# Kernel optimization log

Hardware: AMD Instinct MI355X
Metric: run time of the kernel (lower is better)

The kernel has to match this reference:

```python
import jax, jax.numpy as jnp
import numpy as np

N_HEADS = 16
HIDDEN = 1024
HEAD = HIDDEN // N_HEADS


def setup_inputs() -> dict:
    key = jax.random.key(0)
    ks = jax.random.split(key, 11)
    B, S, H = 2, 2048, HIDDEN
    s = 1.0 / np.sqrt(H)
    return {
        "query": jax.random.normal(ks[0], (B, S, H), jnp.float32),
        "key": jax.random.normal(ks[1], (B, S, H), jnp.float32),
        "value": jax.random.normal(ks[2], (B, S, H), jnp.float32),
        "Wq": jax.random.normal(ks[3], (H, H), jnp.float32) * s,
        "bq": jnp.zeros((H,), jnp.float32),
        "Wk": jax.random.normal(ks[4], (H, H), jnp.float32) * s,
        "bk": jnp.zeros((H,), jnp.float32),
        "Wv": jax.random.normal(ks[5], (H, H), jnp.float32) * s,
        "bv": jnp.zeros((H,), jnp.float32),
        "Wo": jax.random.normal(ks[6], (H, H), jnp.float32) * s,
        "bo": jnp.zeros((H,), jnp.float32),
    }


def reference(query, key, value, Wq, bq, Wk, bk, Wv, bv, Wo, bo):
    B, Sq, H = query.shape
    Sk = key.shape[1]
    # QKV projections, split heads: [B, n_heads, S, head]
    q = (query @ Wq + bq).reshape(B, Sq, N_HEADS, HEAD).transpose(0, 2, 1, 3)
    k = (key @ Wk + bk).reshape(B, Sk, N_HEADS, HEAD).transpose(0, 2, 1, 3)
    v = (value @ Wv + bv).reshape(B, Sk, N_HEADS, HEAD).transpose(0, 2, 1, 3)
    # scaled dot-product attention (no mask, dropout p=0)
    scores = jnp.einsum("bhqd,bhkd->bhqk", q, k) / np.sqrt(HEAD).astype(np.float32)
    attn = jax.nn.softmax(scores, axis=-1)
    out = jnp.einsum("bhqk,bhkd->bhqd", attn, v)
    out = out.transpose(0, 2, 1, 3).reshape(B, Sq, H)
    return out @ Wo + bo
```

## Files before the change

### kernel.cpp

```cpp
#include <hip/hip_runtime.h>
#include <hip/hip_bf16.h>
#include <stdint.h>

typedef unsigned short u16;
typedef short bf16x8 __attribute__((ext_vector_type(8)));
typedef float f32x4 __attribute__((ext_vector_type(4)));

#define DEVI static __device__ __forceinline__

#if __has_builtin(__builtin_amdgcn_exp2f)
#define EXP2F(x) __builtin_amdgcn_exp2f(x)
#else
#define EXP2F(x) exp2f(x)
#endif

DEVI u16 f2bf(float f) {
  union { float f; uint32_t u; } v; v.f = f;
  uint32_t u = v.u;
  u += 0x7fffu + ((u >> 16) & 1u);
  return (u16)(u >> 16);
}
DEVI uint32_t pk2bf(float lo, float hi) {
  __hip_bfloat162 h = __float22bfloat162_rn(float2{lo, hi});
  union { __hip_bfloat162 h; uint32_t u; } v; v.h = h; return v.u;
}

DEVI void async16(const void* g, const void* l) {
  __builtin_amdgcn_global_load_lds(
      (const __attribute__((address_space(1))) void*)g,
      (__attribute__((address_space(3))) void*)l, 16, 0, 0);
}

DEVI f32x4 mfma16(bf16x8 a, bf16x8 b, f32x4 c) {
  return __builtin_amdgcn_mfma_f32_16x16x32_bf16(a, b, c, 0, 0, 0);
}

#define CSC 0.18033688011112042f

__global__ void convx(const float* __restrict__ q, const float* __restrict__ k,
                      const float* __restrict__ v, u16* __restrict__ out) {
  const int z = blockIdx.y;
  const float* src = (z == 0) ? q : (z == 1) ? k : v;
  const int i = (blockIdx.x * 256 + threadIdx.x) * 4;
  float4 f = *(const float4*)(src + i);
  ushort4 o;
  o.x = f2bf(f.x); o.y = f2bf(f.y); o.z = f2bf(f.z); o.w = f2bf(f.w);
  *(ushort4*)(out + (size_t)z * 4194304 + i) = o;
}

__global__ void transw(const float* __restrict__ Wq, const float* __restrict__ Wk,
                       const float* __restrict__ Wv, const float* __restrict__ Wo,
                       u16* __restrict__ WT) {
  __shared__ u16 tile[64 * 68];
  const int z = blockIdx.z;
  const float* W = (z == 0) ? Wq : (z == 1) ? Wk : (z == 2) ? Wv : Wo;
  u16* out = WT + (size_t)z * 1048576;
  const int R0 = blockIdx.y * 64, C0 = blockIdx.x * 64;
  const int t = threadIdx.x;
#pragma unroll
  for (int it = 0; it < 16; ++it) {
    int j = it * 256 + t;
    int r = j >> 6, c = j & 63;
    tile[r * 68 + c] = f2bf(W[(size_t)(R0 + r) * 1024 + C0 + c]);
  }
  __syncthreads();
#pragma unroll
  for (int it = 0; it < 16; ++it) {
    int j = it * 256 + t;
    int c = j >> 6, r = j & 63;
    out[(size_t)(C0 + c) * 1024 + R0 + r] = tile[r * 68 + c];
  }
}

__global__ __launch_bounds__(256, 3)
void qkv_gemm(const u16* __restrict__ XB, const u16* __restrict__ WT,
              const float* __restrict__ bq, const float* __restrict__ bk,
              const float* __restrict__ bv,
              u16* __restrict__ QN, u16* __restrict__ KN, u16* __restrict__ VT) {
  __shared__ u16 smem[16896];
  u16* lA = smem;
  u16* lB = smem + 8192;
  const int z = blockIdx.y;
  const u16* A  = XB + (size_t)z * 4194304;
  const u16* Bt = WT + (size_t)z * 1048576;
  const float* bias = (z == 0) ? bq : (z == 1) ? bk : bv;
  const int T = blockIdx.x;
  const int m0 = (T & 31) * 128, n0 = (T >> 5) * 128;
  const int t = threadIdx.x, lane = t & 63, w = t >> 6;
  const int quad = lane >> 4, l16 = lane & 15;
  const int wm = (w & 1) * 64, wn = (w >> 1) * 64;

  f32x4 acc[4][4] = {};
  for (int kt = 0; kt < 16; ++kt) {
    const int k0 = kt * 64;
#pragma unroll
    for (int it = 0; it < 4; ++it) {
      int i = it * 256 + t;
      int r = i >> 3, cc = i & 7, c = cc ^ (r & 7);
      async16(A + (size_t)(m0 + r) * 1024 + k0 + c * 8, &lA[i * 8]);
      async16(Bt + (size_t)(n0 + r) * 1024 + k0 + c * 8, &lB[i * 8]);
    }
    __syncthreads();
#pragma unroll
    for (int ks = 0; ks < 2; ++ks) {
      bf16x8 af[4], bfr[4];
#pragma unroll
      for (int rt = 0; rt < 4; ++rt) {
        int row = wm + rt * 16 + l16;
        af[rt] = *(const bf16x8*)&lA[row * 64 + ((ks * 4 + quad) ^ (row & 7)) * 8];
      }
#pragma unroll
      for (int ct = 0; ct < 4; ++ct) {
        int row = wn + ct * 16 + l16;
        bfr[ct] = *(const bf16x8*)&lB[row * 64 + ((ks * 4 + quad) ^ (row & 7)) * 8];
      }
#pragma unroll
      for (int rt = 0; rt < 4; ++rt)
#pragma unroll
        for (int ct = 0; ct < 4; ++ct)
          acc[rt][ct] = mfma16(bfr[ct], af[rt], acc[rt][ct]);
    }
    __syncthreads();
  }

  if (z < 2) {
    const float scl = (z == 0) ? CSC : 1.0f;
#pragma unroll
    for (int rt = 0; rt < 4; ++rt) {
      int sl = wm + rt * 16 + l16;
#pragma unroll
      for (int ct = 0; ct < 4; ++ct) {
        int nb = wn + ct * 16 + quad * 4;
        float4 b4 = *(const float4*)&bias[n0 + nb];
        ushort4 pk;
        pk.x = f2bf((acc[rt][ct][0] + b4.x) * scl);
        pk.y = f2bf((acc[rt][ct][1] + b4.y) * scl);
        pk.z = f2bf((acc[rt][ct][2] + b4.z) * scl);
        pk.w = f2bf((acc[rt][ct][3] + b4.w) * scl);
        *(ushort4*)&smem[sl * 132 + nb] = pk;
      }
    }
    __syncthreads();
    u16* out = (z == 0) ? QN : KN;
#pragma unroll
    for (int p = 0; p < 8; ++p) {
      int idx = p * 256 + t;
      int row = idx >> 4, chunk = idx & 15;
      *(bf16x8*)&out[(size_t)(m0 + row) * 1024 + n0 + chunk * 8] =
          *(const bf16x8*)&smem[row * 132 + chunk * 8];
    }
  } else {
#pragma unroll
    for (int rt = 0; rt < 4; ++rt) {
      int sl = wm + rt * 16 + l16;
#pragma unroll
      for (int ct = 0; ct < 4; ++ct) {
        int nb = wn + ct * 16 + quad * 4;
        float4 b4 = *(const float4*)&bias[n0 + nb];
        smem[(nb + 0) * 132 + sl] = f2bf(acc[rt][ct][0] + b4.x);
        smem[(nb + 1) * 132 + sl] = f2bf(acc[rt][ct][1] + b4.y);
        smem[(nb + 2) * 132 + sl] = f2bf(acc[rt][ct][2] + b4.z);
        smem[(nb + 3) * 132 + sl] = f2bf(acc[rt][ct][3] + b4.w);
      }
    }
    __syncthreads();
    const int bb = m0 >> 11, sb = m0 & 2047;
#pragma unroll
    for (int p = 0; p < 8; ++p) {
      int idx = p * 256 + t;
      int dl = idx >> 4, chunk = idx & 15;
      int ncol = n0 + dl, hh = ncol >> 6, dd = ncol & 63;
      *(bf16x8*)&VT[((size_t)((bb * 16 + hh) * 64 + dd)) * 2048 + sb + chunk * 8] =
          *(const bf16x8*)&smem[dl * 132 + chunk * 8];
    }
  }
}

__global__ __launch_bounds__(512, 4)
void attn10(const u16* __restrict__ QN, const u16* __restrict__ KN,
            const u16* __restrict__ VT, u16* __restrict__ AO) {
  __shared__ u16 lK[4][64 * 64];
  __shared__ u16 lV[4][64 * 64];
  const int qt0 = blockIdx.x, h = blockIdx.y, b = blockIdx.z;
  const int t = threadIdx.x, lane = t & 63, w = t >> 6;
  const int quad = lane >> 4, l16 = lane & 15;
  const u16* Qg = QN + ((size_t)(b * 2048 + qt0 * 128)) * 1024 + h * 64;
  const u16* Kg = KN + ((size_t)b * 2048) * 1024 + h * 64;
  const u16* Vg = VT + ((size_t)((b * 16 + h) * 64)) * 2048;

  const int sr_r = t >> 3;
  const int sg_r = (sr_r & 0x23) | ((sr_r & 8) << 1) | ((sr_r & 4) << 1) |
                   ((sr_r & 16) >> 2);
  const int sc_c = (t & 7) ^ (sr_r & 7);

  bf16x8 qf[2];
#pragma unroll
  for (int ks = 0; ks < 2; ++ks)
    qf[ks] = *(const bf16x8*)(Qg + (size_t)(w * 16 + l16) * 1024 + ks * 32 + quad * 8);

  const bf16x8 ones = {0x3F80, 0x3F80, 0x3F80, 0x3F80,
                       0x3F80, 0x3F80, 0x3F80, 0x3F80};

  async16(Kg + (size_t)sg_r * 1024 + sc_c * 8, &lK[0][t * 8]);
  async16(Vg + (size_t)sr_r * 2048 + sc_c * 8, &lV[0][t * 8]);
  async16(Kg + (size_t)(64 + sg_r) * 1024 + sc_c * 8, &lK[1][t * 8]);
  async16(Vg + (size_t)sr_r * 2048 + 64 + sc_c * 8, &lV[1][t * 8]);

  f32x4 o[4] = {};
  f32x4 ls = {};

  for (int kt = 0; kt < 32; ++kt) {
    if (kt + 2 < 32) {
      const int kb = (kt + 2) * 64;
      const int nb2 = (kt + 2) & 3;
      async16(Kg + (size_t)(kb + sg_r) * 1024 + sc_c * 8, &lK[nb2][t * 8]);
      async16(Vg + (size_t)sr_r * 2048 + kb + sc_c * 8, &lV[nb2][t * 8]);
    }
    if (kt < 30)       asm volatile("s_waitcnt vmcnt(4)" ::: "memory");
    else if (kt == 30) asm volatile("s_waitcnt vmcnt(2)" ::: "memory");
    else               asm volatile("s_waitcnt vmcnt(0)" ::: "memory");
    __builtin_amdgcn_s_barrier();
    __builtin_amdgcn_sched_barrier(0);

    const int cur = kt & 3;

    f32x4 sc[4];
    __builtin_amdgcn_s_setprio(1);
#pragma unroll
    for (int st = 0; st < 4; ++st) {
      int row = st * 16 + l16;
      bf16x8 kf0 = *(const bf16x8*)&lK[cur][row * 64 + ((quad) ^ (row & 7)) * 8];
      bf16x8 kf1 = *(const bf16x8*)&lK[cur][row * 64 + ((4 + quad) ^ (row & 7)) * 8];
      f32x4 z = {};
      sc[st] = mfma16(kf0, qf[0], z);
      sc[st] = mfma16(kf1, qf[1], sc[st]);
    }
    __builtin_amdgcn_s_setprio(0);

    union { uint32_t u[4]; bf16x8 v; } pf0c, pf1c;
#pragma unroll
    for (int st = 0; st < 2; ++st) {
      pf0c.u[st * 2 + 0] = pk2bf(EXP2F(sc[st][0]), EXP2F(sc[st][1]));
      pf0c.u[st * 2 + 1] = pk2bf(EXP2F(sc[st][2]), EXP2F(sc[st][3]));
      pf1c.u[st * 2 + 0] = pk2bf(EXP2F(sc[2 + st][0]), EXP2F(sc[2 + st][1]));
      pf1c.u[st * 2 + 1] = pk2bf(EXP2F(sc[2 + st][2]), EXP2F(sc[2 + st][3]));
    }

    __builtin_amdgcn_s_setprio(1);
    ls = mfma16(ones, pf0c.v, ls);
    ls = mfma16(ones, pf1c.v, ls);
#pragma unroll
    for (int dt = 0; dt < 4; ++dt) {
      int row = dt * 16 + l16;
      bf16x8 vf0 = *(const bf16x8*)&lV[cur][row * 64 + ((quad) ^ (row & 7)) * 8];
      bf16x8 vf1 = *(const bf16x8*)&lV[cur][row * 64 + ((4 + quad) ^ (row & 7)) * 8];
      o[dt] = mfma16(vf0, pf0c.v, o[dt]);
      o[dt] = mfma16(vf1, pf1c.v, o[dt]);
    }
    __builtin_amdgcn_s_setprio(0);
  }

  float inv = 1.0f / ls[0];
  int qglob = qt0 * 128 + w * 16 + l16;
  size_t base = ((size_t)(b * 2048 + qglob)) * 1024 + h * 64;
#pragma unroll
  for (int dt = 0; dt < 4; ++dt) {
    ushort4 pk;
    pk.x = f2bf(o[dt][0] * inv);
    pk.y = f2bf(o[dt][1] * inv);
    pk.z = f2bf(o[dt][2] * inv);
    pk.w = f2bf(o[dt][3] * inv);
    *(ushort4*)&AO[base + dt * 16 + quad * 4] = pk;
  }
}

__global__ __launch_bounds__(256, 2)
void oproj_gemm(const u16* __restrict__ AO, const u16* __restrict__ Bt,
                const float* __restrict__ bias, float* __restrict__ out) {
  __shared__ u16 lA[128 * 64];
  __shared__ u16 lB[64 * 64];
  const int T = blockIdx.x;
  const int m0 = (T & 31) * 128, n0 = (T >> 5) * 64;
  const int t = threadIdx.x, lane = t & 63, w = t >> 6;
  const int quad = lane >> 4, l16 = lane & 15;
  const int wm = (w & 1) * 64, wn = (w >> 1) * 32;

  f32x4 acc[4][2] = {};
  for (int kt = 0; kt < 16; ++kt) {
    const int k0 = kt * 64;
#pragma unroll
    for (int it = 0; it < 4; ++it) {
      int i = it * 256 + t;
      int r = i >> 3, cc = i & 7, c = cc ^ (r & 7);
      async16(AO + (size_t)(m0 + r) * 1024 + k0 + c * 8, &lA[i * 8]);
    }
#pragma unroll
    for (int it = 0; it < 2; ++it) {
      int i = it * 256 + t;
      int r = i >> 3, cc = i & 7, c = cc ^ (r & 7);
      async16(Bt + (size_t)(n0 + r) * 1024 + k0 + c * 8, &lB[i * 8]);
    }
    __syncthreads();
#pragma unroll
    for (int ks = 0; ks < 2; ++ks) {
      bf16x8 af[4], bfr[2];
#pragma unroll
      for (int rt = 0; rt < 4; ++rt) {
        int row = wm + rt * 16 + l16;
        af[rt] = *(const bf16x8*)&lA[row * 64 + ((ks * 4 + quad) ^ (row & 7)) * 8];
      }
#pragma unroll
      for (int ct = 0; ct < 2; ++ct) {
        int row = wn + ct * 16 + l16;
        bfr[ct] = *(const bf16x8*)&lB[row * 64 + ((ks * 4 + quad) ^ (row & 7)) * 8];
      }
#pragma unroll
      for (int rt = 0; rt < 4; ++rt)
#pragma unroll
        for (int ct = 0; ct < 2; ++ct)
          acc[rt][ct] = mfma16(af[rt], bfr[ct], acc[rt][ct]);
    }
    __syncthreads();
  }

#pragma unroll
  for (int ct = 0; ct < 2; ++ct) {
    int ncol = n0 + wn + ct * 16 + l16;
    float bvv = bias[ncol];
#pragma unroll
    for (int rt = 0; rt < 4; ++rt)
#pragma unroll
      for (int r = 0; r < 4; ++r) {
        int m = m0 + wm + rt * 16 + quad * 4 + r;
        out[(size_t)m * 1024 + ncol] = acc[rt][ct][r] + bvv;
      }
  }
}

extern "C" void kernel_launch(void* const* d_in, const int* in_sizes, int n_in,
                              void* d_out, int out_size, void* d_ws, size_t ws_size,
                              hipStream_t stream) {
  const float* query = (const float*)d_in[0];
  const float* key   = (const float*)d_in[1];
  const float* value = (const float*)d_in[2];
  const float* Wq = (const float*)d_in[3];
  const float* bq = (const float*)d_in[4];
  const float* Wk = (const float*)d_in[5];
  const float* bk = (const float*)d_in[6];
  const float* Wv = (const float*)d_in[7];
  const float* bv = (const float*)d_in[8];
  const float* Wo = (const float*)d_in[9];
  const float* bo = (const float*)d_in[10];
  float* out = (float*)d_out;

  u16* WT = (u16*)d_ws;
  u16* QN = WT + 4 * 1048576;
  u16* KN = QN + 4194304;
  u16* VT = KN + 4194304;
  u16* XB = VT + 4194304;
  u16* AO = XB;

  convx<<<dim3(4096, 3), 256, 0, stream>>>(query, key, value, XB);
  transw<<<dim3(16, 16, 4), 256, 0, stream>>>(Wq, Wk, Wv, Wo, WT);
  qkv_gemm<<<dim3(256, 3), 256, 0, stream>>>(XB, WT, bq, bk, bv, QN, KN, VT);
  attn10<<<dim3(16, 16, 2), 512, 0, stream>>>(QN, KN, VT, AO);
  oproj_gemm<<<dim3(512), 256, 0, stream>>>(AO, WT + 3 * 1048576, bo, out);
}
```

Before: 205.1 us.

## Process two KV tiles per barrier in attention loop with paired prefetch

Restructures the attention main loop so each iteration handles two 64-key tiles under one barrier. It issues the prefetch for the next two tiles right after a full vmcnt(0) wait, where before it prefetched one tile two steps ahead with partial waits. The aim is to halve the barrier count and give the scheduler more independent MFMA work per step. The cost is more live score registers and less overlap, since each step now waits for all outstanding loads before computing.

```diff
diff --git a/kernel.cpp b/kernel.cpp
--- a/kernel.cpp
+++ b/kernel.cpp
@@ -177,7 +177,7 @@
 }
 
 __global__ __launch_bounds__(512, 4)
-void attn10(const u16* __restrict__ QN, const u16* __restrict__ KN,
+void attn11(const u16* __restrict__ QN, const u16* __restrict__ KN,
             const u16* __restrict__ VT, u16* __restrict__ AO) {
   __shared__ u16 lK[4][64 * 64];
   __shared__ u16 lV[4][64 * 64];
@@ -209,55 +209,62 @@
   f32x4 o[4] = {};
   f32x4 ls = {};
 
-  for (int kt = 0; kt < 32; ++kt) {
-    if (kt + 2 < 32) {
-      const int kb = (kt + 2) * 64;
-      const int nb2 = (kt + 2) & 3;
-      async16(Kg + (size_t)(kb + sg_r) * 1024 + sc_c * 8, &lK[nb2][t * 8]);
-      async16(Vg + (size_t)sr_r * 2048 + kb + sc_c * 8, &lV[nb2][t * 8]);
-    }
-    if (kt < 30)       asm volatile("s_waitcnt vmcnt(4)" ::: "memory");
-    else if (kt == 30) asm volatile("s_waitcnt vmcnt(2)" ::: "memory");
-    else               asm volatile("s_waitcnt vmcnt(0)" ::: "memory");
+  for (int it = 0; it < 16; ++it) {
+    const int ta = it * 2;
+    asm volatile("s_waitcnt vmcnt(0)" ::: "memory");
     __builtin_amdgcn_s_barrier();
     __builtin_amdgcn_sched_barrier(0);
 
-    const int cur = kt & 3;
-
-    f32x4 sc[4];
+    if (it + 1 < 16) {
+      const int kb0 = (ta + 2) * 64, nb0 = (ta + 2) & 3;
+      async16(Kg + (size_t)(kb0 + sg_r) * 1024 + sc_c * 8, &lK[nb0][t * 8]);
+      async16(Vg + (size_t)sr_r * 2048 + kb0 + sc_c * 8, &lV[nb0][t * 8]);
+      const int kb1 = (ta + 3) * 64, nb1 = (ta + 3) & 3;
+      async16(Kg + (size_t)(kb1 + sg_r) * 1024 + sc_c * 8, &lK[nb1][t * 8]);
+      async16(Vg + (size_t)sr_r * 2048 + kb1 + sc_c * 8, &lV[nb1][t * 8]);
+    }
+
+    f32x4 sc2[2][4];
     __builtin_amdgcn_s_setprio(1);
 #pragma unroll
-    for (int st = 0; st < 4; ++st) {
-      int row = st * 16 + l16;
-      bf16x8 kf0 = *(const bf16x8*)&lK[cur][row * 64 + ((quad) ^ (row & 7)) * 8];
-      bf16x8 kf1 = *(const bf16x8*)&lK[cur][row * 64 + ((4 + quad) ^ (row & 7)) * 8];
-      f32x4 z = {};
-      sc[st] = mfma16(kf0, qf[0], z);
-      sc[st] = mfma16(kf1, qf[1], sc[st]);
+    for (int u = 0; u < 2; ++u) {
+      const u16* Kc = &lK[(ta + u) & 3][0];
+#pragma unroll
+      for (int st = 0; st < 4; ++st) {
+        int row = st * 16 + l16;
+        bf16x8 kf0 = *(const bf16x8*)&Kc[row * 64 + ((quad) ^ (row & 7)) * 8];
+        bf16x8 kf1 = *(const bf16x8*)&Kc[row * 64 + ((4 + quad) ^ (row & 7)) * 8];
+        f32x4 z = {};
+        sc2[u][st] = mfma16(kf0, qf[0], z);
+        sc2[u][st] = mfma16(kf1, qf[1], sc2[u][st]);
+      }
     }
     __builtin_amdgcn_s_setprio(0);
 
-    union { uint32_t u[4]; bf16x8 v; } pf0c, pf1c;
-#pragma unroll
-    for (int st = 0; st < 2; ++st) {
-      pf0c.u[st * 2 + 0] = pk2bf(EXP2F(sc[st][0]), EXP2F(sc[st][1]));
-      pf0c.u[st * 2 + 1] = pk2bf(EXP2F(sc[st][2]), EXP2F(sc[st][3]));
-      pf1c.u[st * 2 + 0] = pk2bf(EXP2F(sc[2 + st][0]), EXP2F(sc[2 + st][1]));
-      pf1c.u[st * 2 + 1] = pk2bf(EXP2F(sc[2 + st][2]), EXP2F(sc[2 + st][3]));
-    }
-
-    __builtin_amdgcn_s_setprio(1);
-    ls = mfma16(ones, pf0c.v, ls);
-    ls = mfma16(ones, pf1c.v, ls);
-#pragma unroll
-    for (int dt = 0; dt < 4; ++dt) {
-      int row = dt * 16 + l16;
-      bf16x8 vf0 = *(const bf16x8*)&lV[cur][row * 64 + ((quad) ^ (row & 7)) * 8];
-      bf16x8 vf1 = *(const bf16x8*)&lV[cur][row * 64 + ((4 + quad) ^ (row & 7)) * 8];
-      o[dt] = mfma16(vf0, pf0c.v, o[dt]);
-      o[dt] = mfma16(vf1, pf1c.v, o[dt]);
-    }
-    __builtin_amdgcn_s_setprio(0);
+#pragma unroll
+    for (int u = 0; u < 2; ++u) {
+      union { uint32_t uw[4]; bf16x8 v; } p0, p1;
+#pragma unroll
+      for (int st = 0; st < 2; ++st) {
+        p0.uw[st * 2 + 0] = pk2bf(EXP2F(sc2[u][st][0]), EXP2F(sc2[u][st][1]));
+        p0.uw[st * 2 + 1] = pk2bf(EXP2F(sc2[u][st][2]), EXP2F(sc2[u][st][3]));
+        p1.uw[st * 2 + 0] = pk2bf(EXP2F(sc2[u][2 + st][0]), EXP2F(sc2[u][2 + st][1]));
+        p1.uw[st * 2 + 1] = pk2bf(EXP2F(sc2[u][2 + st][2]), EXP2F(sc2[u][2 + st][3]));
+      }
+      __builtin_amdgcn_s_setprio(1);
+      ls = mfma16(ones, p0.v, ls);
+      ls = mfma16(ones, p1.v, ls);
+      const u16* Vc = &lV[(ta + u) & 3][0];
+#pragma unroll
+      for (int dt = 0; dt < 4; ++dt) {
+        int row = dt * 16 + l16;
+        bf16x8 vf0 = *(const bf16x8*)&Vc[row * 64 + ((quad) ^ (row & 7)) * 8];
+        bf16x8 vf1 = *(const bf16x8*)&Vc[row * 64 + ((4 + quad) ^ (row & 7)) * 8];
+        o[dt] = mfma16(vf0, p0.v, o[dt]);
+        o[dt] = mfma16(vf1, p1.v, o[dt]);
+      }
+      __builtin_amdgcn_s_setprio(0);
+    }
   }
 
   float inv = 1.0f / ls[0];
@@ -363,6 +370,6 @@
   convx<<<dim3(4096, 3), 256, 0, stream>>>(query, key, value, XB);
   transw<<<dim3(16, 16, 4), 256, 0, stream>>>(Wq, Wk, Wv, Wo, WT);
   qkv_gemm<<<dim3(256, 3), 256, 0, stream>>>(XB, WT, bq, bk, bv, QN, KN, VT);
-  attn10<<<dim3(16, 16, 2), 512, 0, stream>>>(QN, KN, VT, AO);
+  attn11<<<dim3(16, 16, 2), 512, 0, stream>>>(QN, KN, VT, AO);
   oproj_gemm<<<dim3(512), 256, 0, stream>>>(AO, WT + 3 * 1048576, bo, out);
 }
```

Result: slower. 214.0 us (+4.4%).

## Give each attention wave two query tiles, halving threads per block

Applied to the files above, without the earlier changes.

The attention kernel now uses 256 threads (4 waves) per block instead of 512, and each wave handles 32 query rows as two 16-row subtiles. Each K and V fragment read from LDS is reused across both subtiles, which halves LDS reads per MFMA. Each thread now issues four async loads per stage, and the wait counts are adjusted to match. The cost is more registers per thread and fewer waves per block to hide latency. Occupancy is set to 2 blocks per CU through launch bounds.

```diff
diff --git a/kernel.cpp b/kernel.cpp
--- a/kernel.cpp
+++ b/kernel.cpp
@@ -176,8 +176,8 @@
   }
 }
 
-__global__ __launch_bounds__(512, 4)
-void attn10(const u16* __restrict__ QN, const u16* __restrict__ KN,
+__global__ __launch_bounds__(256, 2)
+void attn12(const u16* __restrict__ QN, const u16* __restrict__ KN,
             const u16* __restrict__ VT, u16* __restrict__ AO) {
   __shared__ u16 lK[4][64 * 64];
   __shared__ u16 lV[4][64 * 64];
@@ -193,84 +193,111 @@
                    ((sr_r & 16) >> 2);
   const int sc_c = (t & 7) ^ (sr_r & 7);
 
-  bf16x8 qf[2];
-#pragma unroll
-  for (int ks = 0; ks < 2; ++ks)
-    qf[ks] = *(const bf16x8*)(Qg + (size_t)(w * 16 + l16) * 1024 + ks * 32 + quad * 8);
+  bf16x8 qf[2][2];
+#pragma unroll
+  for (int qs = 0; qs < 2; ++qs)
+#pragma unroll
+    for (int ks = 0; ks < 2; ++ks)
+      qf[qs][ks] = *(const bf16x8*)(Qg + (size_t)(w * 32 + qs * 16 + l16) * 1024 +
+                                    ks * 32 + quad * 8);
 
   const bf16x8 ones = {0x3F80, 0x3F80, 0x3F80, 0x3F80,
                        0x3F80, 0x3F80, 0x3F80, 0x3F80};
 
-  async16(Kg + (size_t)sg_r * 1024 + sc_c * 8, &lK[0][t * 8]);
-  async16(Vg + (size_t)sr_r * 2048 + sc_c * 8, &lV[0][t * 8]);
-  async16(Kg + (size_t)(64 + sg_r) * 1024 + sc_c * 8, &lK[1][t * 8]);
-  async16(Vg + (size_t)sr_r * 2048 + 64 + sc_c * 8, &lV[1][t * 8]);
-
-  f32x4 o[4] = {};
-  f32x4 ls = {};
+#define STAGE12(kb, buf)                                                      \
+  do {                                                                        \
+    async16(Kg + (size_t)((kb) + sg_r) * 1024 + sc_c * 8, &lK[buf][t * 8]);   \
+    async16(Kg + (size_t)((kb) + sg_r + 32) * 1024 + sc_c * 8,                \
+            &lK[buf][(t + 256) * 8]);                                         \
+    async16(Vg + (size_t)sr_r * 2048 + (kb) + sc_c * 8, &lV[buf][t * 8]);     \
+    async16(Vg + (size_t)(sr_r + 32) * 2048 + (kb) + sc_c * 8,                \
+            &lV[buf][(t + 256) * 8]);                                         \
+  } while (0)
+
+  STAGE12(0, 0);
+  STAGE12(64, 1);
+
+  f32x4 o[2][4] = {};
+  f32x4 ls0 = {}, ls1 = {};
 
   for (int kt = 0; kt < 32; ++kt) {
     if (kt + 2 < 32) {
       const int kb = (kt + 2) * 64;
-      const int nb2 = (kt + 2) & 3;
-      async16(Kg + (size_t)(kb + sg_r) * 1024 + sc_c * 8, &lK[nb2][t * 8]);
-      async16(Vg + (size_t)sr_r * 2048 + kb + sc_c * 8, &lV[nb2][t * 8]);
-    }
-    if (kt < 30)       asm volatile("s_waitcnt vmcnt(4)" ::: "memory");
-    else if (kt == 30) asm volatile("s_waitcnt vmcnt(2)" ::: "memory");
+      const int nb = (kt + 2) & 3;
+      STAGE12(kb, nb);
+    }
+    if (kt < 30)       asm volatile("s_waitcnt vmcnt(8)" ::: "memory");
+    else if (kt == 30) asm volatile("s_waitcnt vmcnt(4)" ::: "memory");
     else               asm volatile("s_waitcnt vmcnt(0)" ::: "memory");
     __builtin_amdgcn_s_barrier();
     __builtin_amdgcn_sched_barrier(0);
 
     const int cur = kt & 3;
 
-    f32x4 sc[4];
+    f32x4 sc[2][4];
     __builtin_amdgcn_s_setprio(1);
 #pragma unroll
     for (int st = 0; st < 4; ++st) {
       int row = st * 16 + l16;
       bf16x8 kf0 = *(const bf16x8*)&lK[cur][row * 64 + ((quad) ^ (row & 7)) * 8];
       bf16x8 kf1 = *(const bf16x8*)&lK[cur][row * 64 + ((4 + quad) ^ (row & 7)) * 8];
-      f32x4 z = {};
-      sc[st] = mfma16(kf0, qf[0], z);
-      sc[st] = mfma16(kf1, qf[1], sc[st]);
+#pragma unroll
+      for (int qs = 0; qs < 2; ++qs) {
+        f32x4 z = {};
+        sc[qs][st] = mfma16(kf0, qf[qs][0], z);
+        sc[qs][st] = mfma16(kf1, qf[qs][1], sc[qs][st]);
+      }
     }
     __builtin_amdgcn_s_setprio(0);
 
-    union { uint32_t u[4]; bf16x8 v; } pf0c, pf1c;
+    union { uint32_t uw[4]; bf16x8 v; } p00, p01, p10, p11;
 #pragma unroll
     for (int st = 0; st < 2; ++st) {
-      pf0c.u[st * 2 + 0] = pk2bf(EXP2F(sc[st][0]), EXP2F(sc[st][1]));
-      pf0c.u[st * 2 + 1] = pk2bf(EXP2F(sc[st][2]), EXP2F(sc[st][3]));
-      pf1c.u[st * 2 + 0] = pk2bf(EXP2F(sc[2 + st][0]), EXP2F(sc[2 + st][1]));
-      pf1c.u[st * 2 + 1] = pk2bf(EXP2F(sc[2 + st][2]), EXP2F(sc[2 + st][3]));
+      p00.uw[st * 2 + 0] = pk2bf(EXP2F(sc[0][st][0]), EXP2F(sc[0][st][1]));
+      p00.uw[st * 2 + 1] = pk2bf(EXP2F(sc[0][st][2]), EXP2F(sc[0][st][3]));
+      p01.uw[st * 2 + 0] = pk2bf(EXP2F(sc[0][2 + st][0]), EXP2F(sc[0][2 + st][1]));
+      p01.uw[st * 2 + 1] = pk2bf(EXP2F(sc[0][2 + st][2]), EXP2F(sc[0][2 + st][3]));
+      p10.uw[st * 2 + 0] = pk2bf(EXP2F(sc[1][st][0]), EXP2F(sc[1][st][1]));
+      p10.uw[st * 2 + 1] = pk2bf(EXP2F(sc[1][st][2]), EXP2F(sc[1][st][3]));
+      p11.uw[st * 2 + 0] = pk2bf(EXP2F(sc[1][2 + st][0]), EXP2F(sc[1][2 + st][1]));
+      p11.uw[st * 2 + 1] = pk2bf(EXP2F(sc[1][2 + st][2]), EXP2F(sc[1][2 + st][3]));
     }
 
     __builtin_amdgcn_s_setprio(1);
-    ls = mfma16(ones, pf0c.v, ls);
-    ls = mfma16(ones, pf1c.v, ls);
+    ls0 = mfma16(ones, p00.v, ls0);
+    ls0 = mfma16(ones, p01.v, ls0);
+    ls1 = mfma16(ones, p10.v, ls1);
+    ls1 = mfma16(ones, p11.v, ls1);
 #pragma unroll
     for (int dt = 0; dt < 4; ++dt) {
       int row = dt * 16 + l16;
       bf16x8 vf0 = *(const bf16x8*)&lV[cur][row * 64 + ((quad) ^ (row & 7)) * 8];
       bf16x8 vf1 = *(const bf16x8*)&lV[cur][row * 64 + ((4 + quad) ^ (row & 7)) * 8];
-      o[dt] = mfma16(vf0, pf0c.v, o[dt]);
-      o[dt] = mfma16(vf1, pf1c.v, o[dt]);
+      o[0][dt] = mfma16(vf0, p00.v, o[0][dt]);
+      o[0][dt] = mfma16(vf1, p01.v, o[0][dt]);
+      o[1][dt] = mfma16(vf0, p10.v, o[1][dt]);
+      o[1][dt] = mfma16(vf1, p11.v, o[1][dt]);
     }
     __builtin_amdgcn_s_setprio(0);
   }
-
-  float inv = 1.0f / ls[0];
-  int qglob = qt0 * 128 + w * 16 + l16;
-  size_t base = ((size_t)(b * 2048 + qglob)) * 1024 + h * 64;
-#pragma unroll
-  for (int dt = 0; dt < 4; ++dt) {
-    ushort4 pk;
-    pk.x = f2bf(o[dt][0] * inv);
-    pk.y = f2bf(o[dt][1] * inv);
-    pk.z = f2bf(o[dt][2] * inv);
-    pk.w = f2bf(o[dt][3] * inv);
-    *(ushort4*)&AO[base + dt * 16 + quad * 4] = pk;
+#undef STAGE12
+
+  float inv0 = 1.0f / ls0[0];
+  float inv1 = 1.0f / ls1[0];
+#pragma unroll
+  for (int qs = 0; qs < 2; ++qs) {
+    float inv = qs ? inv1 : inv0;
+    int qglob = qt0 * 128 + w * 32 + qs * 16 + l16;
+    size_t base = ((size_t)(b * 2048 + qglob)) * 1024 + h * 64;
+#pragma unroll
+    for (int dt = 0; dt < 4; ++dt) {
+      ushort4 pk;
+      pk.x = f2bf(o[qs][dt][0] * inv);
+      pk.y = f2bf(o[qs][dt][1] * inv);
+      pk.z = f2bf(o[qs][dt][2] * inv);
+      pk.w = f2bf(o[qs][dt][3] * inv);
+      *(ushort4*)&AO[base + dt * 16 + quad * 4] = pk;
+    }
   }
 }
 
@@ -363,6 +390,6 @@
   convx<<<dim3(4096, 3), 256, 0, stream>>>(query, key, value, XB);
   transw<<<dim3(16, 16, 4), 256, 0, stream>>>(Wq, Wk, Wv, Wo, WT);
   qkv_gemm<<<dim3(256, 3), 256, 0, stream>>>(XB, WT, bq, bk, bv, QN, KN, VT);
-  attn10<<<dim3(16, 16, 2), 512, 0, stream>>>(QN, KN, VT, AO);
+  attn12<<<dim3(16, 16, 2), 256, 0, stream>>>(QN, KN, VT, AO);
   oproj_gemm<<<dim3(512), 256, 0, stream>>>(AO, WT + 3 * 1048576, bo, out);
 }
```

Measured after the change: 214.8 us. 4.7% more time.
